# Performance work log

Measured on AMD Instinct MI355X. Metric: run time of the kernel, lower is better.

Reference implementation:

```python
import jax, jax.numpy as jnp
import numpy as np

N = 10000; IN = 256; HID = 256; Z = 64; NC = 10; E = 320000
GAMMA = -0.5; ZETA = 1.1; TEMP = 0.5  # GlobalArgs.gamma/zeta, AttentionFusion.temperature


def _spmm(row, col, vals, x):
    # sparse [N,N] @ dense [N,D] via gather + segment-sum scatter
    return jax.ops.segment_sum(vals[:, None] * x[col], row, num_segments=N)


def _encode(x, row, col, vals, gcn_W, gcn_b, m1_W, m1_b, m2_W, m2_b, s1_W, s1_b, s2_W, s2_b):
    hidden = jax.nn.relu(_spmm(row, col, vals, x @ gcn_W + gcn_b))  # GCNLayer
    mean = jax.nn.relu(hidden @ m1_W + m1_b) @ m2_W + m2_b
    std = jax.nn.softplus(jax.nn.relu(hidden @ s1_W + s1_b) @ s2_W + s2_b)
    return mean, mean, std  # eval mode: z = x_mean


def _denoise(x, row, col, vals, nb_W, nb_b, sf_W, sf_b, att_W, att_b):
    h1 = jax.nn.relu(x[row] @ nb_W + nb_b)  # nblayers_0 on source feats
    h2 = jax.nn.relu(x[col] @ sf_W + sf_b)  # selflayers_0 on dest feats
    w = jnp.concatenate([h1, h2], axis=1) @ att_W + att_b  # [E,1] log_alpha
    gate = jax.nn.sigmoid(w[:, 0])  # eval-mode hard-concrete
    mask = jnp.clip(gate * (ZETA - GAMMA) + GAMMA, 0.0, 1.0)
    mv = vals * mask
    rowsum = jax.ops.segment_sum(mv, row, num_segments=N) + 1e-10
    d = jnp.clip(rowsum ** -0.5, 0.0, 10.0)
    norm_vals = mv * d[row] * d[col]
    l0 = jnp.mean(jax.nn.sigmoid(w - jnp.log(-GAMMA / ZETA)))
    return norm_vals, l0


def setup_inputs() -> dict:
    key = jax.random.key(0)
    ks = jax.random.split(key, 32)
    w = lambda k, s: jax.random.normal(k, s, jnp.float32) * 0.05
    inp = {}
    inp['x'] = jax.random.normal(ks[0], (N, IN), jnp.float32)
    inp['row'] = jax.random.randint(ks[1], (E,), 0, N)
    inp['col'] = jax.random.randint(ks[2], (E,), 0, N)
    inp['adj_vals'] = jax.random.uniform(ks[3], (E,), jnp.float32)
    inp['gcn_W'] = w(ks[4], (IN, HID)); inp['gcn_b'] = jnp.zeros((HID,), jnp.float32)
    inp['m1_W'] = w(ks[5], (HID, Z)); inp['m1_b'] = jnp.zeros((Z,), jnp.float32)
    inp['m2_W'] = w(ks[6], (Z, Z)); inp['m2_b'] = jnp.zeros((Z,), jnp.float32)
    inp['s1_W'] = w(ks[7], (HID, Z)); inp['s1_b'] = jnp.zeros((Z,), jnp.float32)
    inp['s2_W'] = w(ks[8], (Z, Z)); inp['s2_b'] = jnp.zeros((Z,), jnp.float32)
    inp['nb_W'] = w(ks[9], (IN, HID)); inp['nb_b'] = jnp.zeros((HID,), jnp.float32)
    inp['sf_W'] = w(ks[10], (IN, HID)); inp['sf_b'] = jnp.zeros((HID,), jnp.float32)
    inp['att_W'] = w(ks[11], (2 * HID, 1)); inp['att_b'] = jnp.zeros((1,), jnp.float32)
    inp['f1_W'] = w(ks[12], (Z, 32)); inp['f1_b'] = jnp.zeros((32,), jnp.float32)
    inp['f2_W'] = jnp.zeros((32, 1), jnp.float32)  # att[2].weight.fill_(0.0)
    inp['head_W'] = w(ks[13], (Z, NC)); inp['head_b'] = jnp.zeros((NC,), jnp.float32)
    inp['d1_W'] = w(ks[14], (Z, HID)); inp['d1_b'] = jnp.zeros((HID,), jnp.float32)
    inp['d2_W'] = w(ks[15], (HID, IN)); inp['d2_b'] = jnp.zeros((IN,), jnp.float32)
    return inp


def reference(x, row, col, adj_vals, gcn_W, gcn_b, m1_W, m1_b, m2_W, m2_b, s1_W, s1_b, s2_W, s2_b,
              nb_W, nb_b, sf_W, sf_b, att_W, att_b, f1_W, f1_b, f2_W, head_W, head_b,
              d1_W, d1_b, d2_W, d2_b):
    enc = (gcn_W, gcn_b, m1_W, m1_b, m2_W, m2_b, s1_W, s1_b, s2_W, s2_b)
    # generative view
    z_gen, mu, logstd = _encode(x, row, col, adj_vals, *enc)
    adj_logits = z_gen @ z_gen.T  # vgae_decoder
    # denoised view
    den_vals, l0_loss = _denoise(x, row, col, adj_vals, nb_W, nb_b, sf_W, sf_b, att_W, att_b)
    z_den, _, _ = _encode(x, row, col, den_vals, *enc)
    # attention fusion
    h = jnp.stack([z_gen, z_den], axis=1)  # [N,2,Z]
    score = jnp.tanh(h @ f1_W + f1_b) @ f2_W  # [N,2,1]
    weights = jax.nn.softmax(score / TEMP, axis=1)
    z_fused = jnp.sum(h * weights, axis=1)
    # heads (cluster_proj is identity)
    q_fused = jax.nn.softmax(z_fused @ head_W + head_b, axis=1)
    q_gen = jax.nn.softmax(z_gen @ head_W + head_b, axis=1)
    q_den = jax.nn.softmax(z_den @ head_W + head_b, axis=1)
    recon_den = jax.nn.relu(z_den @ d1_W + d1_b) @ d2_W + d2_b
    return (q_fused, q_gen, q_den, adj_logits, z_fused, mu, logstd, l0_loss, z_den, weights, recon_den)
```

## Files before the change

kernel.cpp:

```cpp
#include <hip/hip_runtime.h>
#include <math.h>

#define NN 10000
#define EE 320000

#define OQF  0LL
#define OQG  100000LL
#define OQD  200000LL
#define OADJ 300000LL
#define OZF  100300000LL
#define OMU  100940000LL
#define OLS  101580000LL
#define OL0  102220000LL
#define OZD  102220001LL
#define OWT  102860001LL
#define OREC 102880001LL

typedef short short8 __attribute__((ext_vector_type(8)));
typedef float f32x4 __attribute__((ext_vector_type(4)));

static __device__ __forceinline__ ushort f2bf(float f) {
  uint u = __float_as_uint(f);
  return (ushort)((u + 0x7fffu + ((u >> 16) & 1u)) >> 16);
}

__global__ __launch_bounds__(256) void k_prep(
    const float* __restrict__ x,
    const float* __restrict__ gcnW, const float* __restrict__ nbW,
    const float* __restrict__ sfW, const float* __restrict__ d2W,
    const float* __restrict__ d1W, const float* __restrict__ m1W,
    const float* __restrict__ s1W, const float* __restrict__ m2W,
    const float* __restrict__ s2W,
    ushort* __restrict__ XB,
    ushort* __restrict__ GWT, ushort* __restrict__ NWT, ushort* __restrict__ SWT,
    ushort* __restrict__ D2T, ushort* __restrict__ D1T, ushort* __restrict__ M1T,
    ushort* __restrict__ S1T, ushort* __restrict__ M2T, ushort* __restrict__ S2T)
{
  const int b = blockIdx.x, tid = threadIdx.x;
  if (b < 2500) {
    const int i = b * 1024 + tid * 4;
    const float4 v = *(const float4*)(x + i);
    ushort4 u;
    u.x = f2bf(v.x); u.y = f2bf(v.y); u.z = f2bf(v.z); u.w = f2bf(v.w);
    *(ushort4*)(XB + i) = u;
    return;
  }
  const int t2 = b - 2500;
  if (t2 < 1024) {
    const int m = t2 >> 8, n = t2 & 255;
    const float* src = (m == 0) ? gcnW : (m == 1) ? nbW : (m == 2) ? sfW : d2W;
    ushort* dst = (m == 0) ? GWT : (m == 1) ? NWT : (m == 2) ? SWT : D2T;
    dst[n * 256 + tid] = f2bf(src[tid * 256 + n]);
  } else if (t2 < 1088) {
    const int local = (t2 - 1024) * 256 + tid;
    const int n = local >> 6, k = local & 63;
    D1T[local] = f2bf(d1W[k * 256 + n]);
  } else if (t2 < 1152) {
    const int n = t2 - 1088;
    M1T[n * 256 + tid] = f2bf(m1W[tid * 64 + n]);
  } else if (t2 < 1216) {
    const int n = t2 - 1152;
    S1T[n * 256 + tid] = f2bf(s1W[tid * 64 + n]);
  } else if (t2 < 1232) {
    const int local = (t2 - 1216) * 256 + tid;
    const int n = local >> 6, k = local & 63;
    M2T[local] = f2bf(m2W[k * 64 + n]);
  } else {
    const int local = (t2 - 1232) * 256 + tid;
    const int n = local >> 6, k = local & 63;
    S2T[local] = f2bf(s2W[k * 64 + n]);
  }
}

__global__ __launch_bounds__(256) void k_gin(
    const ushort* __restrict__ XB,
    const ushort* __restrict__ GWT, const ushort* __restrict__ NWT,
    const ushort* __restrict__ SWT,
    const float* __restrict__ gcnb, const float* __restrict__ nbb,
    const float* __restrict__ sfb, const float* __restrict__ attW,
    ushort* __restrict__ xwb, float* __restrict__ a1, float* __restrict__ a2)
{
  const int sel = blockIdx.y;
  const ushort* WT = (sel == 0) ? GWT : (sel == 1) ? NWT : SWT;
  const float* B = (sel == 0) ? gcnb : (sel == 1) ? nbb : sfb;
  const float* redw = attW + ((sel == 2) ? 256 : 0);
  float* redout = (sel == 1) ? a1 : a2;

  const int tid = threadIdx.x;
  const int wave = tid >> 6, lane = tid & 63;
  const int lr = lane & 15, lk = lane >> 4;
  const int i0 = blockIdx.x * 64;
  const int j0 = wave * 64;

  f32x4 acc[4][4];
#pragma unroll
  for (int ti = 0; ti < 4; ++ti)
#pragma unroll
    for (int tj = 0; tj < 4; ++tj) acc[ti][tj] = (f32x4){0.f, 0.f, 0.f, 0.f};

  const short8 z8 = {0, 0, 0, 0, 0, 0, 0, 0};
  for (int kk = 0; kk < 8; ++kk) {
    short8 a[4], bfr[4];
#pragma unroll
    for (int t = 0; t < 4; ++t) {
      const int ri = i0 + t * 16 + lr;
      a[t] = (ri < NN) ? *(const short8*)(XB + (size_t)ri * 256 + kk * 32 + lk * 8) : z8;
      bfr[t] = *(const short8*)(WT + (size_t)(j0 + t * 16 + lr) * 256 + kk * 32 + lk * 8);
    }
#pragma unroll
    for (int ti = 0; ti < 4; ++ti)
#pragma unroll
      for (int tj = 0; tj < 4; ++tj)
        acc[ti][tj] = __builtin_amdgcn_mfma_f32_16x16x32_bf16(a[ti], bfr[tj], acc[ti][tj], 0, 0, 0);
  }

  if (sel == 0) {
#pragma unroll
    for (int ti = 0; ti < 4; ++ti) {
      const int gi0 = i0 + ti * 16 + lk * 4;
#pragma unroll
      for (int tj = 0; tj < 4; ++tj) {
        const int gj = j0 + tj * 16 + lr;
        const float bv = B[gj];
#pragma unroll
        for (int r = 0; r < 4; ++r) {
          const int gi = gi0 + r;
          if (gi < NN) xwb[(size_t)gi * 256 + gj] = f2bf(acc[ti][tj][r] + bv);
        }
      }
    }
  } else {
    float bw[4], aw[4];
#pragma unroll
    for (int tj = 0; tj < 4; ++tj) {
      const int gj = j0 + tj * 16 + lr;
      bw[tj] = B[gj];
      aw[tj] = redw[gj];
    }
#pragma unroll
    for (int ti = 0; ti < 4; ++ti) {
      const int gi0 = i0 + ti * 16 + lk * 4;
#pragma unroll
      for (int r = 0; r < 4; ++r) {
        float s = 0.f;
#pragma unroll
        for (int tj = 0; tj < 4; ++tj)
          s += fmaxf(acc[ti][tj][r] + bw[tj], 0.f) * aw[tj];
#pragma unroll
        for (int m = 1; m < 16; m <<= 1) s += __shfl_xor(s, m, 64);
        const int gi = gi0 + r;
        if (lr == 0 && gi < NN) atomicAdd(&redout[gi], s);
      }
    }
  }
}

__global__ __launch_bounds__(256) void k_denoise(
    const int* __restrict__ row, const int* __restrict__ col,
    const float* __restrict__ vals, const float* __restrict__ a1,
    const float* __restrict__ a2, const float* __restrict__ attb,
    float4* __restrict__ bk, int* __restrict__ cnt, float* __restrict__ l0acc)
{
  const int e = blockIdx.x * 256 + threadIdx.x;
  const int r = row[e], c = col[e];
  const float w = a1[r] + a2[c] + attb[0];
  const float gate = 1.f / (1.f + expf(-w));
  const float mask = fminf(fmaxf(gate * 1.6f - 0.5f, 0.f), 1.f);
  const float m = vals[e] * mask;
  const int p = atomicAdd(&cnt[r], 1);
  if (p < 64) bk[(size_t)r * 64 + p] = make_float4(__int_as_float(c), vals[e], m, 0.f);
  float part = 1.f / (1.f + expf(-(w + 0.78845736f)));
#pragma unroll
  for (int off = 32; off > 0; off >>= 1) part += __shfl_down(part, off);
  __shared__ float sw[4];
  if ((threadIdx.x & 63) == 0) sw[threadIdx.x >> 6] = part;
  __syncthreads();
  if (threadIdx.x == 0) atomicAdd(l0acc, sw[0] + sw[1] + sw[2] + sw[3]);
}

__global__ __launch_bounds__(256) void k_dinv(
    const float4* __restrict__ bk, const int* __restrict__ cnt,
    float* __restrict__ dinv)
{
  const int tid = threadIdx.x;
  const int r = blockIdx.x * 4 + (tid >> 6);
  const int lane = tid & 63;
  if (r >= NN) return;
  const int m = min(cnt[r], 64);
  float s = (lane < m) ? bk[(size_t)r * 64 + lane].z : 0.f;
#pragma unroll
  for (int off = 32; off > 0; off >>= 1) s += __shfl_xor(s, off, 64);
  if (lane == 0) dinv[r] = fminf(rsqrtf(s + 1e-10f), 10.f);
}

__global__ __launch_bounds__(256) void k_spmm(
    const ushort* __restrict__ xwb, const float4* __restrict__ bk,
    const int* __restrict__ cnt, const float* __restrict__ dinv,
    ushort* __restrict__ h1, ushort* __restrict__ h2)
{
  const int tid = threadIdx.x;
  const int n = blockIdx.x * 2 + (tid >> 7);
  const int c = tid & 127;
  const int m = min(cnt[n], 64);
  const float dr = dinv[n];
  const float4* b = bk + (size_t)n * 64;
  float a10 = 0.f, a11 = 0.f, a20 = 0.f, a21 = 0.f;
  float b10 = 0.f, b11 = 0.f, b20 = 0.f, b21 = 0.f;
  int i = 0;
  for (; i + 2 <= m; i += 2) {
    const float4 e0 = b[i], e1 = b[i + 1];
    const int c0 = __float_as_int(e0.x), c1 = __float_as_int(e1.x);
    const uint u0 = *(const uint*)(xwb + (size_t)c0 * 256 + 2 * c);
    const uint u1 = *(const uint*)(xwb + (size_t)c1 * 256 + 2 * c);
    const float d0 = dr * dinv[c0] * e0.z;
    const float d1 = dr * dinv[c1] * e1.z;
    const float v00 = __uint_as_float(u0 << 16), v01 = __uint_as_float(u0 & 0xffff0000u);
    const float v10 = __uint_as_float(u1 << 16), v11 = __uint_as_float(u1 & 0xffff0000u);
    a10 = fmaf(e0.y, v00, a10); a11 = fmaf(e0.y, v01, a11);
    a20 = fmaf(d0, v00, a20);   a21 = fmaf(d0, v01, a21);
    b10 = fmaf(e1.y, v10, b10); b11 = fmaf(e1.y, v11, b11);
    b20 = fmaf(d1, v10, b20);   b21 = fmaf(d1, v11, b21);
  }
  if (i < m) {
    const float4 e0 = b[i];
    const int c0 = __float_as_int(e0.x);
    const uint u0 = *(const uint*)(xwb + (size_t)c0 * 256 + 2 * c);
    const float d0 = dr * dinv[c0] * e0.z;
    const float v00 = __uint_as_float(u0 << 16), v01 = __uint_as_float(u0 & 0xffff0000u);
    a10 = fmaf(e0.y, v00, a10); a11 = fmaf(e0.y, v01, a11);
    a20 = fmaf(d0, v00, a20);   a21 = fmaf(d0, v01, a21);
  }
  a10 += b10; a11 += b11; a20 += b20; a21 += b21;
  const uint p1 = (uint)f2bf(fmaxf(a10, 0.f)) | ((uint)f2bf(fmaxf(a11, 0.f)) << 16);
  const uint p2 = (uint)f2bf(fmaxf(a20, 0.f)) | ((uint)f2bf(fmaxf(a21, 0.f)) << 16);
  *(uint*)(h1 + (size_t)n * 256 + 2 * c) = p1;
  *(uint*)(h2 + (size_t)n * 256 + 2 * c) = p2;
}

__global__ __launch_bounds__(128) void k_tail(
    const ushort* __restrict__ H1B, const ushort* __restrict__ H2B,
    const ushort* __restrict__ M1T, const ushort* __restrict__ S1T,
    const ushort* __restrict__ M2T, const ushort* __restrict__ S2T,
    const float* __restrict__ m1b, const float* __restrict__ m2b,
    const float* __restrict__ s1b, const float* __restrict__ s2b,
    float* __restrict__ out, float* __restrict__ zden,
    ushort* __restrict__ zbg, ushort* __restrict__ zbd)
{
  const int v = blockIdx.y;
  const ushort* A   = (v == 2) ? H2B : H1B;
  const ushort* W1T = (v == 1) ? S1T : M1T;
  const float*  B1  = (v == 1) ? s1b : m1b;
  const ushort* W2T = (v == 1) ? S2T : M2T;
  const float*  B2  = (v == 1) ? s2b : m2b;

  __shared__ ushort Ts[128][72];
  const int tid = threadIdx.x;
  const int wave = tid >> 6, lane = tid & 63;
  const int lr = lane & 15, lk = lane >> 4;
  const int i0 = blockIdx.x * 128 + wave * 64;
  const short8 z8 = {0, 0, 0, 0, 0, 0, 0, 0};

  f32x4 acc[4][4];
#pragma unroll
  for (int ti = 0; ti < 4; ++ti)
#pragma unroll
    for (int tj = 0; tj < 4; ++tj) acc[ti][tj] = (f32x4){0.f, 0.f, 0.f, 0.f};
  for (int kk = 0; kk < 8; ++kk) {
    short8 a[4], bfr[4];
#pragma unroll
    for (int t = 0; t < 4; ++t) {
      const int ri = i0 + t * 16 + lr;
      a[t] = (ri < NN) ? *(const short8*)(A + (size_t)ri * 256 + kk * 32 + lk * 8) : z8;
      bfr[t] = *(const short8*)(W1T + (size_t)(t * 16 + lr) * 256 + kk * 32 + lk * 8);
    }
#pragma unroll
    for (int ti = 0; ti < 4; ++ti)
#pragma unroll
      for (int tj = 0; tj < 4; ++tj)
        acc[ti][tj] = __builtin_amdgcn_mfma_f32_16x16x32_bf16(a[ti], bfr[tj], acc[ti][tj], 0, 0, 0);
  }
#pragma unroll
  for (int ti = 0; ti < 4; ++ti) {
#pragma unroll
    for (int tj = 0; tj < 4; ++tj) {
      const int cl = tj * 16 + lr;
      const float b1 = B1[cl];
#pragma unroll
      for (int r = 0; r < 4; ++r) {
        const int lrow = wave * 64 + ti * 16 + lk * 4 + r;
        Ts[lrow][cl] = f2bf(fmaxf(acc[ti][tj][r] + b1, 0.f));
      }
    }
  }
  __syncthreads();
  f32x4 acc2[4][4];
#pragma unroll
  for (int ti = 0; ti < 4; ++ti)
#pragma unroll
    for (int tj = 0; tj < 4; ++tj) acc2[ti][tj] = (f32x4){0.f, 0.f, 0.f, 0.f};
  for (int kk = 0; kk < 2; ++kk) {
    short8 a[4], bfr[4];
#pragma unroll
    for (int t = 0; t < 4; ++t) {
      a[t] = *(const short8*)(&Ts[wave * 64 + t * 16 + lr][kk * 32 + lk * 8]);
      bfr[t] = *(const short8*)(W2T + (size_t)(t * 16 + lr) * 64 + kk * 32 + lk * 8);
    }
#pragma unroll
    for (int ti = 0; ti < 4; ++ti)
#pragma unroll
      for (int tj = 0; tj < 4; ++tj)
        acc2[ti][tj] = __builtin_amdgcn_mfma_f32_16x16x32_bf16(a[ti], bfr[tj], acc2[ti][tj], 0, 0, 0);
  }
#pragma unroll
  for (int ti = 0; ti < 4; ++ti) {
    const int gi0 = i0 + ti * 16 + lk * 4;
#pragma unroll
    for (int tj = 0; tj < 4; ++tj) {
      const int gj = tj * 16 + lr;
      const float bv = B2[gj];
#pragma unroll
      for (int r = 0; r < 4; ++r) {
        const int gi = gi0 + r;
        if (gi >= NN) continue;
        float t = acc2[ti][tj][r] + bv;
        if (v == 0) {
          out[OMU + (size_t)gi * 64 + gj] = t;
          zbg[(size_t)gi * 64 + gj] = f2bf(t);
        } else if (v == 1) {
          t = (t > 20.f) ? t : log1pf(expf(t));
          out[OLS + (size_t)gi * 64 + gj] = t;
        } else {
          zden[(size_t)gi * 64 + gj] = t;
          out[OZD + (size_t)gi * 64 + gj] = t;
          zbd[(size_t)gi * 64 + gj] = f2bf(t);
        }
      }
    }
  }
}

__global__ __launch_bounds__(256) void k_post(
    const ushort* __restrict__ ZBG, const ushort* __restrict__ ZBD,
    const float* __restrict__ ZDENW,
    const ushort* __restrict__ D1T, const float* __restrict__ d1b,
    const ushort* __restrict__ D2T, const float* __restrict__ d2b,
    const float* __restrict__ f1W, const float* __restrict__ f1b,
    const float* __restrict__ f2W,
    const float* __restrict__ hW, const float* __restrict__ hb,
    const float* __restrict__ l0acc, float* __restrict__ out)
{
  __shared__ char smraw[64 * 264 * 2];
  const int b = blockIdx.x;
  const int tid = threadIdx.x;
  const short8 z8 = {0, 0, 0, 0, 0, 0, 0, 0};

  if (b < 157) {
    ushort* HS = (ushort*)smraw;
    const int wave = tid >> 6, lane = tid & 63;
    const int lr = lane & 15, lk = lane >> 4;
    const int i0 = b * 64;
    const int j0 = wave * 64;
    f32x4 acc[4][4];
#pragma unroll
    for (int ti = 0; ti < 4; ++ti)
#pragma unroll
      for (int tj = 0; tj < 4; ++tj) acc[ti][tj] = (f32x4){0.f, 0.f, 0.f, 0.f};
    for (int kk = 0; kk < 2; ++kk) {
      short8 a[4], bfr[4];
#pragma unroll
      for (int t = 0; t < 4; ++t) {
        const int ri = i0 + t * 16 + lr;
        a[t] = (ri < NN) ? *(const short8*)(ZBD + (size_t)ri * 64 + kk * 32 + lk * 8) : z8;
        bfr[t] = *(const short8*)(D1T + (size_t)(j0 + t * 16 + lr) * 64 + kk * 32 + lk * 8);
      }
#pragma unroll
      for (int ti = 0; ti < 4; ++ti)
#pragma unroll
        for (int tj = 0; tj < 4; ++tj)
          acc[ti][tj] = __builtin_amdgcn_mfma_f32_16x16x32_bf16(a[ti], bfr[tj], acc[ti][tj], 0, 0, 0);
    }
#pragma unroll
    for (int ti = 0; ti < 4; ++ti) {
      const int rl0 = ti * 16 + lk * 4;
#pragma unroll
      for (int tj = 0; tj < 4; ++tj) {
        const int cl = j0 + tj * 16 + lr;
        const float bv = d1b[cl];
#pragma unroll
        for (int r = 0; r < 4; ++r)
          HS[(rl0 + r) * 264 + cl] = f2bf(fmaxf(acc[ti][tj][r] + bv, 0.f));
      }
    }
    __syncthreads();
#pragma unroll
    for (int ti = 0; ti < 4; ++ti)
#pragma unroll
      for (int tj = 0; tj < 4; ++tj) acc[ti][tj] = (f32x4){0.f, 0.f, 0.f, 0.f};
    for (int kk = 0; kk < 8; ++kk) {
      short8 a[4], bfr[4];
#pragma unroll
      for (int t = 0; t < 4; ++t) {
        a[t] = *(const short8*)(HS + (t * 16 + lr) * 264 + kk * 32 + lk * 8);
        bfr[t] = *(const short8*)(D2T + (size_t)(j0 + t * 16 + lr) * 256 + kk * 32 + lk * 8);
      }
#pragma unroll
      for (int ti = 0; ti < 4; ++ti)
#pragma unroll
        for (int tj = 0; tj < 4; ++tj)
          acc[ti][tj] = __builtin_amdgcn_mfma_f32_16x16x32_bf16(a[ti], bfr[tj], acc[ti][tj], 0, 0, 0);
    }
#pragma unroll
    for (int ti = 0; ti < 4; ++ti) {
      const int gi0 = i0 + ti * 16 + lk * 4;
#pragma unroll
      for (int tj = 0; tj < 4; ++tj) {
        const int gj = j0 + tj * 16 + lr;
        const float bv = d2b[gj];
#pragma unroll
        for (int r = 0; r < 4; ++r) {
          const int gi = gi0 + r;
          if (gi < NN) out[OREC + (size_t)gi * 256 + gj] = acc[ti][tj][r] + bv;
        }
      }
    }
  } else if (b < 197) {
    const int n = (b - 157) * 256 + tid;
    if (n == 0) out[OL0] = l0acc[0] * (1.f / (float)EE);
    if (n >= NN) return;
    const float* zg = out + OMU + (size_t)n * 64;
    const float* zdn = ZDENW + (size_t)n * 64;
    float ag[32], ad[32];
#pragma unroll
    for (int c2 = 0; c2 < 32; ++c2) { const float bb = f1b[c2]; ag[c2] = bb; ad[c2] = bb; }
    for (int l = 0; l < 64; ++l) {
      const float a = zg[l];
      const float d = zdn[l];
#pragma unroll
      for (int c2 = 0; c2 < 32; ++c2) {
        const float w = f1W[l * 32 + c2];
        ag[c2] = fmaf(a, w, ag[c2]);
        ad[c2] = fmaf(d, w, ad[c2]);
      }
    }
    float sg = 0.f, sd = 0.f;
#pragma unroll
    for (int c2 = 0; c2 < 32; ++c2) {
      sg += tanhf(ag[c2]) * f2W[c2];
      sd += tanhf(ad[c2]) * f2W[c2];
    }
    const float e0 = sg * 2.f, e1 = sd * 2.f;
    const float m = fmaxf(e0, e1);
    float w0 = expf(e0 - m), w1 = expf(e1 - m);
    const float inv = 1.f / (w0 + w1);
    w0 *= inv; w1 *= inv;
    float lgf[10], lgg[10], lgd[10];
#pragma unroll
    for (int c = 0; c < 10; ++c) { const float bb = hb[c]; lgf[c] = bb; lgg[c] = bb; lgd[c] = bb; }
    for (int l = 0; l < 64; ++l) {
      const float zgv = zg[l], zdv = zdn[l];
      const float zfv = w0 * zgv + w1 * zdv;
      out[OZF + (size_t)n * 64 + l] = zfv;
#pragma unroll
      for (int c = 0; c < 10; ++c) {
        const float w = hW[l * 10 + c];
        lgf[c] = fmaf(zfv, w, lgf[c]);
        lgg[c] = fmaf(zgv, w, lgg[c]);
        lgd[c] = fmaf(zdv, w, lgd[c]);
      }
    }
#pragma unroll
    for (int h = 0; h < 3; ++h) {
      float* lg = (h == 0) ? lgf : (h == 1) ? lgg : lgd;
      float* q = out + ((h == 0) ? OQF : (h == 1) ? OQG : OQD) + (size_t)n * 10;
      float mm = lg[0];
#pragma unroll
      for (int c = 1; c < 10; ++c) mm = fmaxf(mm, lg[c]);
      float s = 0.f;
#pragma unroll
      for (int c = 0; c < 10; ++c) { lg[c] = expf(lg[c] - mm); s += lg[c]; }
      const float invq = 1.f / s;
#pragma unroll
      for (int c = 0; c < 10; ++c) q[c] = lg[c] * invq;
    }
    out[OWT + (size_t)n * 2 + 0] = w0;
    out[OWT + (size_t)n * 2 + 1] = w1;
  } else {
    const int bb = b - 197;
    const int bi = bb / 79, bj = bb % 79;
    const int wave = tid >> 6, lane = tid & 63;
    const int lr = lane & 15, lk = lane >> 4;
    const int i0 = bi * 128 + (wave >> 1) * 64;
    const int j0 = bj * 128 + (wave & 1) * 64;
    float* zs = (float*)smraw + wave * (16 * 76);
    short8 a[4][2], bfr[4][2];
#pragma unroll
    for (int t = 0; t < 4; ++t) {
      const int ri = i0 + t * 16 + lr;
      const int rj = j0 + t * 16 + lr;
#pragma unroll
      for (int kk = 0; kk < 2; ++kk) {
        a[t][kk] = (ri < NN) ? *(const short8*)(ZBG + (size_t)ri * 64 + kk * 32 + lk * 8) : z8;
        bfr[t][kk] = (rj < NN) ? *(const short8*)(ZBG + (size_t)rj * 64 + kk * 32 + lk * 8) : z8;
      }
    }
    f32x4 acc[4][4];
#pragma unroll
    for (int ti = 0; ti < 4; ++ti)
#pragma unroll
      for (int tj = 0; tj < 4; ++tj) {
        acc[ti][tj] = (f32x4){0.f, 0.f, 0.f, 0.f};
        acc[ti][tj] = __builtin_amdgcn_mfma_f32_16x16x32_bf16(a[ti][0], bfr[tj][0], acc[ti][tj], 0, 0, 0);
        acc[ti][tj] = __builtin_amdgcn_mfma_f32_16x16x32_bf16(a[ti][1], bfr[tj][1], acc[ti][tj], 0, 0, 0);
      }
#pragma unroll
    for (int ti = 0; ti < 4; ++ti) {
#pragma unroll
      for (int tj = 0; tj < 4; ++tj)
#pragma unroll
        for (int r = 0; r < 4; ++r)
          zs[(lk * 4 + r) * 76 + tj * 16 + lr] = acc[ti][tj][r];
#pragma unroll
      for (int s = 0; s < 4; ++s) {
        const int rrow = (s & 1) * 8 + (lane >> 3);
        const int ccol = (s >> 1) * 32 + (lane & 7) * 4;
        const int gi = i0 + ti * 16 + rrow;
        const int gj = j0 + ccol;
        if (gi < NN && gj < NN) {
          float4 v;
          v.x = zs[rrow * 76 + ccol + 0];
          v.y = zs[rrow * 76 + ccol + 1];
          v.z = zs[rrow * 76 + ccol + 2];
          v.w = zs[rrow * 76 + ccol + 3];
          *(float4*)(out + OADJ + (size_t)gi * NN + gj) = v;
        }
      }
    }
  }
}

extern "C" void kernel_launch(void* const* d_in, const int* in_sizes, int n_in,
                              void* d_out, int out_size, void* d_ws, size_t ws_size,
                              hipStream_t stream)
{
  const float* x     = (const float*)d_in[0];
  const int*   row   = (const int*)d_in[1];
  const int*   col   = (const int*)d_in[2];
  const float* avals = (const float*)d_in[3];
  const float* gcnW  = (const float*)d_in[4];
  const float* gcnb  = (const float*)d_in[5];
  const float* m1W   = (const float*)d_in[6];
  const float* m1b   = (const float*)d_in[7];
  const float* m2W   = (const float*)d_in[8];
  const float* m2b   = (const float*)d_in[9];
  const float* s1W   = (const float*)d_in[10];
  const float* s1b   = (const float*)d_in[11];
  const float* s2W   = (const float*)d_in[12];
  const float* s2b   = (const float*)d_in[13];
  const float* nbW   = (const float*)d_in[14];
  const float* nbb   = (const float*)d_in[15];
  const float* sfW   = (const float*)d_in[16];
  const float* sfb   = (const float*)d_in[17];
  const float* attW  = (const float*)d_in[18];
  const float* attb  = (const float*)d_in[19];
  const float* f1W   = (const float*)d_in[20];
  const float* f1b   = (const float*)d_in[21];
  const float* f2W   = (const float*)d_in[22];
  const float* headW = (const float*)d_in[23];
  const float* headb = (const float*)d_in[24];
  const float* d1W   = (const float*)d_in[25];
  const float* d1b   = (const float*)d_in[26];
  const float* d2W   = (const float*)d_in[27];
  const float* d2b   = (const float*)d_in[28];
  float* out = (float*)d_out;

  float* ws = (float*)d_ws;
  size_t o = 0;
  float4* BK   = (float4*)(ws + o); o += (size_t)NN * 64 * 4;
  ushort* XB   = (ushort*)(ws + o); o += (size_t)NN * 128;
  ushort* XWB  = (ushort*)(ws + o); o += (size_t)NN * 128;
  ushort* GWT  = (ushort*)(ws + o); o += 32768;
  ushort* NWT  = (ushort*)(ws + o); o += 32768;
  ushort* SWT  = (ushort*)(ws + o); o += 32768;
  ushort* D2T  = (ushort*)(ws + o); o += 32768;
  ushort* D1T  = (ushort*)(ws + o); o += 8192;
  ushort* M1T  = (ushort*)(ws + o); o += 8192;
  ushort* S1T  = (ushort*)(ws + o); o += 8192;
  ushort* M2T  = (ushort*)(ws + o); o += 2048;
  ushort* S2T  = (ushort*)(ws + o); o += 2048;
  ushort* H1B  = (ushort*)(ws + o); o += (size_t)NN * 128;
  ushort* H2B  = (ushort*)(ws + o); o += (size_t)NN * 128;
  float* ZDENW = ws + o; o += (size_t)NN * 64;
  ushort* ZBG  = (ushort*)(ws + o); o += (size_t)NN * 32;
  ushort* ZBD  = (ushort*)(ws + o); o += (size_t)NN * 32;
  float* DINV  = ws + o; o += NN;
  const size_t zoff = o;
  float* A1    = ws + o; o += NN;
  float* A2    = ws + o; o += NN;
  int*   CNT   = (int*)(ws + o); o += NN;
  float* L0A   = ws + o; o += 1;

  hipMemsetAsync((void*)(ws + zoff), 0, (o - zoff) * sizeof(float), stream);

  k_prep<<<3748, 256, 0, stream>>>(x, gcnW, nbW, sfW, d2W, d1W, m1W, s1W, m2W, s2W,
                                   XB, GWT, NWT, SWT, D2T, D1T, M1T, S1T, M2T, S2T);
  k_gin<<<dim3(157, 3), 256, 0, stream>>>(XB, GWT, NWT, SWT, gcnb, nbb, sfb, attW, XWB, A1, A2);
  k_denoise<<<EE / 256, 256, 0, stream>>>(row, col, avals, A1, A2, attb, BK, CNT, L0A);
  k_dinv<<<2500, 256, 0, stream>>>(BK, CNT, DINV);
  k_spmm<<<NN / 2, 256, 0, stream>>>(XWB, BK, CNT, DINV, H1B, H2B);
  k_tail<<<dim3(79, 3), 128, 0, stream>>>(H1B, H2B, M1T, S1T, M2T, S2T,
                                          m1b, m2b, s1b, s2b, out, ZDENW, ZBG, ZBD);
  k_post<<<6438, 256, 0, stream>>>(ZBG, ZBD, ZDENW, D1T, d1b, D2T, d2b,
                                   f1W, f1b, f2W, headW, headb, L0A, out);
}
```

Before: 283.0 us.

## Fuse all stages into one persistent kernel with grid-wide barriers

Replaces the seven separate kernel launches with a single persistent kernel of 512 blocks that loops over each stage's virtual blocks and separates stages with an atomic-counter grid barrier. The aim is to remove per-launch overhead and the idle tails between dependent kernels. In exchange, each stage is limited to 512 resident blocks, spin-wait barriers add their own cost, and correctness depends on all 512 blocks being co-resident.

```diff
diff --git a/kernel.cpp b/kernel.cpp
--- a/kernel.cpp
+++ b/kernel.cpp
@@ -3,6 +3,7 @@
 
 #define NN 10000
 #define EE 320000
+#define NB 512
 
 #define OQF  0LL
 #define OQG  100000LL
@@ -24,374 +25,99 @@
   return (ushort)((u + 0x7fffu + ((u >> 16) & 1u)) >> 16);
 }
 
-__global__ __launch_bounds__(256) void k_prep(
-    const float* __restrict__ x,
-    const float* __restrict__ gcnW, const float* __restrict__ nbW,
-    const float* __restrict__ sfW, const float* __restrict__ d2W,
-    const float* __restrict__ d1W, const float* __restrict__ m1W,
-    const float* __restrict__ s1W, const float* __restrict__ m2W,
-    const float* __restrict__ s2W,
-    ushort* __restrict__ XB,
+static __device__ __forceinline__ void gbar(int* ctr) {
+  __syncthreads();
+  if (threadIdx.x == 0) {
+    __threadfence();
+    __hip_atomic_fetch_add(ctr, 1, __ATOMIC_ACQ_REL, __HIP_MEMORY_SCOPE_AGENT);
+    while (__hip_atomic_load(ctr, __ATOMIC_ACQUIRE, __HIP_MEMORY_SCOPE_AGENT) < NB) {
+      __builtin_amdgcn_s_sleep(1);
+    }
+    __threadfence();
+  }
+  __syncthreads();
+}
+
+__global__ __launch_bounds__(256, 2) void k_fused(
+    const float* __restrict__ x, const int* __restrict__ row,
+    const int* __restrict__ col, const float* __restrict__ avals,
+    const float* __restrict__ gcnW, const float* __restrict__ gcnb,
+    const float* __restrict__ m1W, const float* __restrict__ m1b,
+    const float* __restrict__ m2W, const float* __restrict__ m2b,
+    const float* __restrict__ s1W, const float* __restrict__ s1b,
+    const float* __restrict__ s2W, const float* __restrict__ s2b,
+    const float* __restrict__ nbW, const float* __restrict__ nbb,
+    const float* __restrict__ sfW, const float* __restrict__ sfb,
+    const float* __restrict__ attW, const float* __restrict__ attb,
+    const float* __restrict__ f1W, const float* __restrict__ f1b,
+    const float* __restrict__ f2W, const float* __restrict__ hW,
+    const float* __restrict__ hb,
+    const float* __restrict__ d1W, const float* __restrict__ d1b,
+    const float* __restrict__ d2W, const float* __restrict__ d2b,
+    float* __restrict__ out,
+    float4* __restrict__ BK, ushort* __restrict__ XB, ushort* __restrict__ XWB,
     ushort* __restrict__ GWT, ushort* __restrict__ NWT, ushort* __restrict__ SWT,
     ushort* __restrict__ D2T, ushort* __restrict__ D1T, ushort* __restrict__ M1T,
-    ushort* __restrict__ S1T, ushort* __restrict__ M2T, ushort* __restrict__ S2T)
+    ushort* __restrict__ S1T, ushort* __restrict__ M2T, ushort* __restrict__ S2T,
+    ushort* __restrict__ H1B, ushort* __restrict__ H2B,
+    float* __restrict__ ZDENW, ushort* __restrict__ ZBG, ushort* __restrict__ ZBD,
+    float* __restrict__ DINV, float* __restrict__ A1, float* __restrict__ A2,
+    int* __restrict__ CNT, float* __restrict__ L0A, int* __restrict__ BAR)
 {
-  const int b = blockIdx.x, tid = threadIdx.x;
-  if (b < 2500) {
-    const int i = b * 1024 + tid * 4;
-    const float4 v = *(const float4*)(x + i);
-    ushort4 u;
-    u.x = f2bf(v.x); u.y = f2bf(v.y); u.z = f2bf(v.z); u.w = f2bf(v.w);
-    *(ushort4*)(XB + i) = u;
-    return;
-  }
-  const int t2 = b - 2500;
-  if (t2 < 1024) {
-    const int m = t2 >> 8, n = t2 & 255;
-    const float* src = (m == 0) ? gcnW : (m == 1) ? nbW : (m == 2) ? sfW : d2W;
-    ushort* dst = (m == 0) ? GWT : (m == 1) ? NWT : (m == 2) ? SWT : D2T;
-    dst[n * 256 + tid] = f2bf(src[tid * 256 + n]);
-  } else if (t2 < 1088) {
-    const int local = (t2 - 1024) * 256 + tid;
-    const int n = local >> 6, k = local & 63;
-    D1T[local] = f2bf(d1W[k * 256 + n]);
-  } else if (t2 < 1152) {
-    const int n = t2 - 1088;
-    M1T[n * 256 + tid] = f2bf(m1W[tid * 64 + n]);
-  } else if (t2 < 1216) {
-    const int n = t2 - 1152;
-    S1T[n * 256 + tid] = f2bf(s1W[tid * 64 + n]);
-  } else if (t2 < 1232) {
-    const int local = (t2 - 1216) * 256 + tid;
-    const int n = local >> 6, k = local & 63;
-    M2T[local] = f2bf(m2W[k * 64 + n]);
-  } else {
-    const int local = (t2 - 1232) * 256 + tid;
-    const int n = local >> 6, k = local & 63;
-    S2T[local] = f2bf(s2W[k * 64 + n]);
-  }
-}
-
-__global__ __launch_bounds__(256) void k_gin(
-    const ushort* __restrict__ XB,
-    const ushort* __restrict__ GWT, const ushort* __restrict__ NWT,
-    const ushort* __restrict__ SWT,
-    const float* __restrict__ gcnb, const float* __restrict__ nbb,
-    const float* __restrict__ sfb, const float* __restrict__ attW,
-    ushort* __restrict__ xwb, float* __restrict__ a1, float* __restrict__ a2)
-{
-  const int sel = blockIdx.y;
-  const ushort* WT = (sel == 0) ? GWT : (sel == 1) ? NWT : SWT;
-  const float* B = (sel == 0) ? gcnb : (sel == 1) ? nbb : sfb;
-  const float* redw = attW + ((sel == 2) ? 256 : 0);
-  float* redout = (sel == 1) ? a1 : a2;
-
-  const int tid = threadIdx.x;
-  const int wave = tid >> 6, lane = tid & 63;
-  const int lr = lane & 15, lk = lane >> 4;
-  const int i0 = blockIdx.x * 64;
-  const int j0 = wave * 64;
-
-  f32x4 acc[4][4];
-#pragma unroll
-  for (int ti = 0; ti < 4; ++ti)
-#pragma unroll
-    for (int tj = 0; tj < 4; ++tj) acc[ti][tj] = (f32x4){0.f, 0.f, 0.f, 0.f};
-
-  const short8 z8 = {0, 0, 0, 0, 0, 0, 0, 0};
-  for (int kk = 0; kk < 8; ++kk) {
-    short8 a[4], bfr[4];
-#pragma unroll
-    for (int t = 0; t < 4; ++t) {
-      const int ri = i0 + t * 16 + lr;
-      a[t] = (ri < NN) ? *(const short8*)(XB + (size_t)ri * 256 + kk * 32 + lk * 8) : z8;
-      bfr[t] = *(const short8*)(WT + (size_t)(j0 + t * 16 + lr) * 256 + kk * 32 + lk * 8);
-    }
-#pragma unroll
-    for (int ti = 0; ti < 4; ++ti)
-#pragma unroll
-      for (int tj = 0; tj < 4; ++tj)
-        acc[ti][tj] = __builtin_amdgcn_mfma_f32_16x16x32_bf16(a[ti], bfr[tj], acc[ti][tj], 0, 0, 0);
-  }
-
-  if (sel == 0) {
-#pragma unroll
-    for (int ti = 0; ti < 4; ++ti) {
-      const int gi0 = i0 + ti * 16 + lk * 4;
-#pragma unroll
-      for (int tj = 0; tj < 4; ++tj) {
-        const int gj = j0 + tj * 16 + lr;
-        const float bv = B[gj];
-#pragma unroll
-        for (int r = 0; r < 4; ++r) {
-          const int gi = gi0 + r;
-          if (gi < NN) xwb[(size_t)gi * 256 + gj] = f2bf(acc[ti][tj][r] + bv);
-        }
-      }
-    }
-  } else {
-    float bw[4], aw[4];
-#pragma unroll
-    for (int tj = 0; tj < 4; ++tj) {
-      const int gj = j0 + tj * 16 + lr;
-      bw[tj] = B[gj];
-      aw[tj] = redw[gj];
-    }
-#pragma unroll
-    for (int ti = 0; ti < 4; ++ti) {
-      const int gi0 = i0 + ti * 16 + lk * 4;
-#pragma unroll
-      for (int r = 0; r < 4; ++r) {
-        float s = 0.f;
-#pragma unroll
-        for (int tj = 0; tj < 4; ++tj)
-          s += fmaxf(acc[ti][tj][r] + bw[tj], 0.f) * aw[tj];
-#pragma unroll
-        for (int m = 1; m < 16; m <<= 1) s += __shfl_xor(s, m, 64);
-        const int gi = gi0 + r;
-        if (lr == 0 && gi < NN) atomicAdd(&redout[gi], s);
-      }
-    }
-  }
-}
-
-__global__ __launch_bounds__(256) void k_denoise(
-    const int* __restrict__ row, const int* __restrict__ col,
-    const float* __restrict__ vals, const float* __restrict__ a1,
-    const float* __restrict__ a2, const float* __restrict__ attb,
-    float4* __restrict__ bk, int* __restrict__ cnt, float* __restrict__ l0acc)
-{
-  const int e = blockIdx.x * 256 + threadIdx.x;
-  const int r = row[e], c = col[e];
-  const float w = a1[r] + a2[c] + attb[0];
-  const float gate = 1.f / (1.f + expf(-w));
-  const float mask = fminf(fmaxf(gate * 1.6f - 0.5f, 0.f), 1.f);
-  const float m = vals[e] * mask;
-  const int p = atomicAdd(&cnt[r], 1);
-  if (p < 64) bk[(size_t)r * 64 + p] = make_float4(__int_as_float(c), vals[e], m, 0.f);
-  float part = 1.f / (1.f + expf(-(w + 0.78845736f)));
-#pragma unroll
-  for (int off = 32; off > 0; off >>= 1) part += __shfl_down(part, off);
+  __shared__ char smraw[256 * 72 * 2];
   __shared__ float sw[4];
-  if ((threadIdx.x & 63) == 0) sw[threadIdx.x >> 6] = part;
-  __syncthreads();
-  if (threadIdx.x == 0) atomicAdd(l0acc, sw[0] + sw[1] + sw[2] + sw[3]);
-}
-
-__global__ __launch_bounds__(256) void k_dinv(
-    const float4* __restrict__ bk, const int* __restrict__ cnt,
-    float* __restrict__ dinv)
-{
-  const int tid = threadIdx.x;
-  const int r = blockIdx.x * 4 + (tid >> 6);
-  const int lane = tid & 63;
-  if (r >= NN) return;
-  const int m = min(cnt[r], 64);
-  float s = (lane < m) ? bk[(size_t)r * 64 + lane].z : 0.f;
-#pragma unroll
-  for (int off = 32; off > 0; off >>= 1) s += __shfl_xor(s, off, 64);
-  if (lane == 0) dinv[r] = fminf(rsqrtf(s + 1e-10f), 10.f);
-}
-
-__global__ __launch_bounds__(256) void k_spmm(
-    const ushort* __restrict__ xwb, const float4* __restrict__ bk,
-    const int* __restrict__ cnt, const float* __restrict__ dinv,
-    ushort* __restrict__ h1, ushort* __restrict__ h2)
-{
-  const int tid = threadIdx.x;
-  const int n = blockIdx.x * 2 + (tid >> 7);
-  const int c = tid & 127;
-  const int m = min(cnt[n], 64);
-  const float dr = dinv[n];
-  const float4* b = bk + (size_t)n * 64;
-  float a10 = 0.f, a11 = 0.f, a20 = 0.f, a21 = 0.f;
-  float b10 = 0.f, b11 = 0.f, b20 = 0.f, b21 = 0.f;
-  int i = 0;
-  for (; i + 2 <= m; i += 2) {
-    const float4 e0 = b[i], e1 = b[i + 1];
-    const int c0 = __float_as_int(e0.x), c1 = __float_as_int(e1.x);
-    const uint u0 = *(const uint*)(xwb + (size_t)c0 * 256 + 2 * c);
-    const uint u1 = *(const uint*)(xwb + (size_t)c1 * 256 + 2 * c);
-    const float d0 = dr * dinv[c0] * e0.z;
-    const float d1 = dr * dinv[c1] * e1.z;
-    const float v00 = __uint_as_float(u0 << 16), v01 = __uint_as_float(u0 & 0xffff0000u);
-    const float v10 = __uint_as_float(u1 << 16), v11 = __uint_as_float(u1 & 0xffff0000u);
-    a10 = fmaf(e0.y, v00, a10); a11 = fmaf(e0.y, v01, a11);
-    a20 = fmaf(d0, v00, a20);   a21 = fmaf(d0, v01, a21);
-    b10 = fmaf(e1.y, v10, b10); b11 = fmaf(e1.y, v11, b11);
-    b20 = fmaf(d1, v10, b20);   b21 = fmaf(d1, v11, b21);
-  }
-  if (i < m) {
-    const float4 e0 = b[i];
-    const int c0 = __float_as_int(e0.x);
-    const uint u0 = *(const uint*)(xwb + (size_t)c0 * 256 + 2 * c);
-    const float d0 = dr * dinv[c0] * e0.z;
-    const float v00 = __uint_as_float(u0 << 16), v01 = __uint_as_float(u0 & 0xffff0000u);
-    a10 = fmaf(e0.y, v00, a10); a11 = fmaf(e0.y, v01, a11);
-    a20 = fmaf(d0, v00, a20);   a21 = fmaf(d0, v01, a21);
-  }
-  a10 += b10; a11 += b11; a20 += b20; a21 += b21;
-  const uint p1 = (uint)f2bf(fmaxf(a10, 0.f)) | ((uint)f2bf(fmaxf(a11, 0.f)) << 16);
-  const uint p2 = (uint)f2bf(fmaxf(a20, 0.f)) | ((uint)f2bf(fmaxf(a21, 0.f)) << 16);
-  *(uint*)(h1 + (size_t)n * 256 + 2 * c) = p1;
-  *(uint*)(h2 + (size_t)n * 256 + 2 * c) = p2;
-}
-
-__global__ __launch_bounds__(128) void k_tail(
-    const ushort* __restrict__ H1B, const ushort* __restrict__ H2B,
-    const ushort* __restrict__ M1T, const ushort* __restrict__ S1T,
-    const ushort* __restrict__ M2T, const ushort* __restrict__ S2T,
-    const float* __restrict__ m1b, const float* __restrict__ m2b,
-    const float* __restrict__ s1b, const float* __restrict__ s2b,
-    float* __restrict__ out, float* __restrict__ zden,
-    ushort* __restrict__ zbg, ushort* __restrict__ zbd)
-{
-  const int v = blockIdx.y;
-  const ushort* A   = (v == 2) ? H2B : H1B;
-  const ushort* W1T = (v == 1) ? S1T : M1T;
-  const float*  B1  = (v == 1) ? s1b : m1b;
-  const ushort* W2T = (v == 1) ? S2T : M2T;
-  const float*  B2  = (v == 1) ? s2b : m2b;
-
-  __shared__ ushort Ts[128][72];
-  const int tid = threadIdx.x;
-  const int wave = tid >> 6, lane = tid & 63;
-  const int lr = lane & 15, lk = lane >> 4;
-  const int i0 = blockIdx.x * 128 + wave * 64;
-  const short8 z8 = {0, 0, 0, 0, 0, 0, 0, 0};
-
-  f32x4 acc[4][4];
-#pragma unroll
-  for (int ti = 0; ti < 4; ++ti)
-#pragma unroll
-    for (int tj = 0; tj < 4; ++tj) acc[ti][tj] = (f32x4){0.f, 0.f, 0.f, 0.f};
-  for (int kk = 0; kk < 8; ++kk) {
-    short8 a[4], bfr[4];
-#pragma unroll
-    for (int t = 0; t < 4; ++t) {
-      const int ri = i0 + t * 16 + lr;
-      a[t] = (ri < NN) ? *(const short8*)(A + (size_t)ri * 256 + kk * 32 + lk * 8) : z8;
-      bfr[t] = *(const short8*)(W1T + (size_t)(t * 16 + lr) * 256 + kk * 32 + lk * 8);
-    }
-#pragma unroll
-    for (int ti = 0; ti < 4; ++ti)
-#pragma unroll
-      for (int tj = 0; tj < 4; ++tj)
-        acc[ti][tj] = __builtin_amdgcn_mfma_f32_16x16x32_bf16(a[ti], bfr[tj], acc[ti][tj], 0, 0, 0);
-  }
-#pragma unroll
-  for (int ti = 0; ti < 4; ++ti) {
-#pragma unroll
-    for (int tj = 0; tj < 4; ++tj) {
-      const int cl = tj * 16 + lr;
-      const float b1 = B1[cl];
-#pragma unroll
-      for (int r = 0; r < 4; ++r) {
-        const int lrow = wave * 64 + ti * 16 + lk * 4 + r;
-        Ts[lrow][cl] = f2bf(fmaxf(acc[ti][tj][r] + b1, 0.f));
-      }
-    }
-  }
-  __syncthreads();
-  f32x4 acc2[4][4];
-#pragma unroll
-  for (int ti = 0; ti < 4; ++ti)
-#pragma unroll
-    for (int tj = 0; tj < 4; ++tj) acc2[ti][tj] = (f32x4){0.f, 0.f, 0.f, 0.f};
-  for (int kk = 0; kk < 2; ++kk) {
-    short8 a[4], bfr[4];
-#pragma unroll
-    for (int t = 0; t < 4; ++t) {
-      a[t] = *(const short8*)(&Ts[wave * 64 + t * 16 + lr][kk * 32 + lk * 8]);
-      bfr[t] = *(const short8*)(W2T + (size_t)(t * 16 + lr) * 64 + kk * 32 + lk * 8);
-    }
-#pragma unroll
-    for (int ti = 0; ti < 4; ++ti)
-#pragma unroll
-      for (int tj = 0; tj < 4; ++tj)
-        acc2[ti][tj] = __builtin_amdgcn_mfma_f32_16x16x32_bf16(a[ti], bfr[tj], acc2[ti][tj], 0, 0, 0);
-  }
-#pragma unroll
-  for (int ti = 0; ti < 4; ++ti) {
-    const int gi0 = i0 + ti * 16 + lk * 4;
-#pragma unroll
-    for (int tj = 0; tj < 4; ++tj) {
-      const int gj = tj * 16 + lr;
-      const float bv = B2[gj];
-#pragma unroll
-      for (int r = 0; r < 4; ++r) {
-        const int gi = gi0 + r;
-        if (gi >= NN) continue;
-        float t = acc2[ti][tj][r] + bv;
-        if (v == 0) {
-          out[OMU + (size_t)gi * 64 + gj] = t;
-          zbg[(size_t)gi * 64 + gj] = f2bf(t);
-        } else if (v == 1) {
-          t = (t > 20.f) ? t : log1pf(expf(t));
-          out[OLS + (size_t)gi * 64 + gj] = t;
-        } else {
-          zden[(size_t)gi * 64 + gj] = t;
-          out[OZD + (size_t)gi * 64 + gj] = t;
-          zbd[(size_t)gi * 64 + gj] = f2bf(t);
-        }
-      }
-    }
-  }
-}
-
-__global__ __launch_bounds__(256) void k_post(
-    const ushort* __restrict__ ZBG, const ushort* __restrict__ ZBD,
-    const float* __restrict__ ZDENW,
-    const ushort* __restrict__ D1T, const float* __restrict__ d1b,
-    const ushort* __restrict__ D2T, const float* __restrict__ d2b,
-    const float* __restrict__ f1W, const float* __restrict__ f1b,
-    const float* __restrict__ f2W,
-    const float* __restrict__ hW, const float* __restrict__ hb,
-    const float* __restrict__ l0acc, float* __restrict__ out)
-{
-  __shared__ char smraw[64 * 264 * 2];
-  const int b = blockIdx.x;
+  const int bid = blockIdx.x;
   const int tid = threadIdx.x;
   const short8 z8 = {0, 0, 0, 0, 0, 0, 0, 0};
 
-  if (b < 157) {
-    ushort* HS = (ushort*)smraw;
+  for (int vb = bid; vb < 3748; vb += NB) {
+    if (vb < 2500) {
+      const int i = vb * 1024 + tid * 4;
+      const float4 v = *(const float4*)(x + i);
+      ushort4 u;
+      u.x = f2bf(v.x); u.y = f2bf(v.y); u.z = f2bf(v.z); u.w = f2bf(v.w);
+      *(ushort4*)(XB + i) = u;
+      continue;
+    }
+    const int t2 = vb - 2500;
+    if (t2 < 1024) {
+      const int m = t2 >> 8, n = t2 & 255;
+      const float* src = (m == 0) ? gcnW : (m == 1) ? nbW : (m == 2) ? sfW : d2W;
+      ushort* dst = (m == 0) ? GWT : (m == 1) ? NWT : (m == 2) ? SWT : D2T;
+      dst[n * 256 + tid] = f2bf(src[tid * 256 + n]);
+    } else if (t2 < 1088) {
+      const int local = (t2 - 1024) * 256 + tid;
+      const int n = local >> 6, k = local & 63;
+      D1T[local] = f2bf(d1W[k * 256 + n]);
+    } else if (t2 < 1152) {
+      const int n = t2 - 1088;
+      M1T[n * 256 + tid] = f2bf(m1W[tid * 64 + n]);
+    } else if (t2 < 1216) {
+      const int n = t2 - 1152;
+      S1T[n * 256 + tid] = f2bf(s1W[tid * 64 + n]);
+    } else if (t2 < 1232) {
+      const int local = (t2 - 1216) * 256 + tid;
+      const int n = local >> 6, k = local & 63;
+      M2T[local] = f2bf(m2W[k * 64 + n]);
+    } else {
+      const int local = (t2 - 1232) * 256 + tid;
+      const int n = local >> 6, k = local & 63;
+      S2T[local] = f2bf(s2W[k * 64 + n]);
+    }
+  }
+  gbar(BAR + 0);
+
+  for (int vb = bid; vb < 471; vb += NB) {
+    const int bx = vb % 157, sel = vb / 157;
+    const ushort* WT = (sel == 0) ? GWT : (sel == 1) ? NWT : SWT;
+    const float* B = (sel == 0) ? gcnb : (sel == 1) ? nbb : sfb;
+    const float* redw = attW + ((sel == 2) ? 256 : 0);
+    float* redout = (sel == 1) ? A1 : A2;
     const int wave = tid >> 6, lane = tid & 63;
     const int lr = lane & 15, lk = lane >> 4;
-    const int i0 = b * 64;
+    const int i0 = bx * 64;
     const int j0 = wave * 64;
     f32x4 acc[4][4];
-#pragma unroll
-    for (int ti = 0; ti < 4; ++ti)
-#pragma unroll
-      for (int tj = 0; tj < 4; ++tj) acc[ti][tj] = (f32x4){0.f, 0.f, 0.f, 0.f};
-    for (int kk = 0; kk < 2; ++kk) {
-      short8 a[4], bfr[4];
-#pragma unroll
-      for (int t = 0; t < 4; ++t) {
-        const int ri = i0 + t * 16 + lr;
-        a[t] = (ri < NN) ? *(const short8*)(ZBD + (size_t)ri * 64 + kk * 32 + lk * 8) : z8;
-        bfr[t] = *(const short8*)(D1T + (size_t)(j0 + t * 16 + lr) * 64 + kk * 32 + lk * 8);
-      }
-#pragma unroll
-      for (int ti = 0; ti < 4; ++ti)
-#pragma unroll
-        for (int tj = 0; tj < 4; ++tj)
-          acc[ti][tj] = __builtin_amdgcn_mfma_f32_16x16x32_bf16(a[ti], bfr[tj], acc[ti][tj], 0, 0, 0);
-    }
-#pragma unroll
-    for (int ti = 0; ti < 4; ++ti) {
-      const int rl0 = ti * 16 + lk * 4;
-#pragma unroll
-      for (int tj = 0; tj < 4; ++tj) {
-        const int cl = j0 + tj * 16 + lr;
-        const float bv = d1b[cl];
-#pragma unroll
-        for (int r = 0; r < 4; ++r)
-          HS[(rl0 + r) * 264 + cl] = f2bf(fmaxf(acc[ti][tj][r] + bv, 0.f));
-      }
-    }
-    __syncthreads();
 #pragma unroll
     for (int ti = 0; ti < 4; ++ti)
 #pragma unroll
@@ -400,8 +126,9 @@
       short8 a[4], bfr[4];
 #pragma unroll
       for (int t = 0; t < 4; ++t) {
-        a[t] = *(const short8*)(HS + (t * 16 + lr) * 264 + kk * 32 + lk * 8);
-        bfr[t] = *(const short8*)(D2T + (size_t)(j0 + t * 16 + lr) * 256 + kk * 32 + lk * 8);
+        const int ri = i0 + t * 16 + lr;
+        a[t] = (ri < NN) ? *(const short8*)(XB + (size_t)ri * 256 + kk * 32 + lk * 8) : z8;
+        bfr[t] = *(const short8*)(WT + (size_t)(j0 + t * 16 + lr) * 256 + kk * 32 + lk * 8);
       }
 #pragma unroll
       for (int ti = 0; ti < 4; ++ti)
@@ -409,129 +136,394 @@
         for (int tj = 0; tj < 4; ++tj)
           acc[ti][tj] = __builtin_amdgcn_mfma_f32_16x16x32_bf16(a[ti], bfr[tj], acc[ti][tj], 0, 0, 0);
     }
+    if (sel == 0) {
+#pragma unroll
+      for (int ti = 0; ti < 4; ++ti) {
+        const int gi0 = i0 + ti * 16 + lk * 4;
+#pragma unroll
+        for (int tj = 0; tj < 4; ++tj) {
+          const int gj = j0 + tj * 16 + lr;
+          const float bv = B[gj];
+#pragma unroll
+          for (int r = 0; r < 4; ++r) {
+            const int gi = gi0 + r;
+            if (gi < NN) XWB[(size_t)gi * 256 + gj] = f2bf(acc[ti][tj][r] + bv);
+          }
+        }
+      }
+    } else {
+      float bw[4], aw[4];
+#pragma unroll
+      for (int tj = 0; tj < 4; ++tj) {
+        const int gj = j0 + tj * 16 + lr;
+        bw[tj] = B[gj];
+        aw[tj] = redw[gj];
+      }
+#pragma unroll
+      for (int ti = 0; ti < 4; ++ti) {
+        const int gi0 = i0 + ti * 16 + lk * 4;
+#pragma unroll
+        for (int r = 0; r < 4; ++r) {
+          float s = 0.f;
+#pragma unroll
+          for (int tj = 0; tj < 4; ++tj)
+            s += fmaxf(acc[ti][tj][r] + bw[tj], 0.f) * aw[tj];
+#pragma unroll
+          for (int m = 1; m < 16; m <<= 1) s += __shfl_xor(s, m, 64);
+          const int gi = gi0 + r;
+          if (lr == 0 && gi < NN) atomicAdd(&redout[gi], s);
+        }
+      }
+    }
+  }
+  gbar(BAR + 1);
+
+  for (int vb = bid; vb < 1250; vb += NB) {
+    const int e = vb * 256 + tid;
+    const int r = row[e], c = col[e];
+    const float w = A1[r] + A2[c] + attb[0];
+    const float gate = 1.f / (1.f + expf(-w));
+    const float mask = fminf(fmaxf(gate * 1.6f - 0.5f, 0.f), 1.f);
+    const float m = avals[e] * mask;
+    const int p = atomicAdd(&CNT[r], 1);
+    if (p < 64) BK[(size_t)r * 64 + p] = make_float4(__int_as_float(c), avals[e], m, 0.f);
+    float part = 1.f / (1.f + expf(-(w + 0.78845736f)));
+#pragma unroll
+    for (int off = 32; off > 0; off >>= 1) part += __shfl_down(part, off);
+    if ((tid & 63) == 0) sw[tid >> 6] = part;
+    __syncthreads();
+    if (tid == 0) atomicAdd(L0A, sw[0] + sw[1] + sw[2] + sw[3]);
+    __syncthreads();
+  }
+  gbar(BAR + 2);
+
+  for (int vb = bid; vb < 2500; vb += NB) {
+    const int r = vb * 4 + (tid >> 6);
+    const int lane = tid & 63;
+    if (r < NN) {
+      const int m = min(CNT[r], 64);
+      float s = (lane < m) ? BK[(size_t)r * 64 + lane].z : 0.f;
+#pragma unroll
+      for (int off = 32; off > 0; off >>= 1) s += __shfl_xor(s, off, 64);
+      if (lane == 0) DINV[r] = fminf(rsqrtf(s + 1e-10f), 10.f);
+    }
+  }
+  gbar(BAR + 3);
+
+  for (int vb = bid; vb < 5000; vb += NB) {
+    const int n = vb * 2 + (tid >> 7);
+    const int c = tid & 127;
+    const int m = min(CNT[n], 64);
+    const float dr = DINV[n];
+    const float4* b = BK + (size_t)n * 64;
+    float a10 = 0.f, a11 = 0.f, a20 = 0.f, a21 = 0.f;
+    float b10 = 0.f, b11 = 0.f, b20 = 0.f, b21 = 0.f;
+    int i = 0;
+    for (; i + 2 <= m; i += 2) {
+      const float4 e0 = b[i], e1 = b[i + 1];
+      const int c0 = __float_as_int(e0.x), c1 = __float_as_int(e1.x);
+      const uint u0 = *(const uint*)(XWB + (size_t)c0 * 256 + 2 * c);
+      const uint u1 = *(const uint*)(XWB + (size_t)c1 * 256 + 2 * c);
+      const float d0 = dr * DINV[c0] * e0.z;
+      const float d1 = dr * DINV[c1] * e1.z;
+      const float v00 = __uint_as_float(u0 << 16), v01 = __uint_as_float(u0 & 0xffff0000u);
+      const float v10 = __uint_as_float(u1 << 16), v11 = __uint_as_float(u1 & 0xffff0000u);
+      a10 = fmaf(e0.y, v00, a10); a11 = fmaf(e0.y, v01, a11);
+      a20 = fmaf(d0, v00, a20);   a21 = fmaf(d0, v01, a21);
+      b10 = fmaf(e1.y, v10, b10); b11 = fmaf(e1.y, v11, b11);
+      b20 = fmaf(d1, v10, b20);   b21 = fmaf(d1, v11, b21);
+    }
+    if (i < m) {
+      const float4 e0 = b[i];
+      const int c0 = __float_as_int(e0.x);
+      const uint u0 = *(const uint*)(XWB + (size_t)c0 * 256 + 2 * c);
+      const float d0 = dr * DINV[c0] * e0.z;
+      const float v00 = __uint_as_float(u0 << 16), v01 = __uint_as_float(u0 & 0xffff0000u);
+      a10 = fmaf(e0.y, v00, a10); a11 = fmaf(e0.y, v01, a11);
+      a20 = fmaf(d0, v00, a20);   a21 = fmaf(d0, v01, a21);
+    }
+    a10 += b10; a11 += b11; a20 += b20; a21 += b21;
+    const uint p1 = (uint)f2bf(fmaxf(a10, 0.f)) | ((uint)f2bf(fmaxf(a11, 0.f)) << 16);
+    const uint p2 = (uint)f2bf(fmaxf(a20, 0.f)) | ((uint)f2bf(fmaxf(a21, 0.f)) << 16);
+    *(uint*)(H1B + (size_t)n * 256 + 2 * c) = p1;
+    *(uint*)(H2B + (size_t)n * 256 + 2 * c) = p2;
+  }
+  gbar(BAR + 4);
+
+  for (int vb = bid; vb < 120; vb += NB) {
+    const int bx = vb % 40, v = vb / 40;
+    const ushort* A   = (v == 2) ? H2B : H1B;
+    const ushort* W1T = (v == 1) ? S1T : M1T;
+    const float*  B1  = (v == 1) ? s1b : m1b;
+    const ushort* W2T = (v == 1) ? S2T : M2T;
+    const float*  B2  = (v == 1) ? s2b : m2b;
+    ushort* Ts = (ushort*)smraw;
+    const int wave = tid >> 6, lane = tid & 63;
+    const int lr = lane & 15, lk = lane >> 4;
+    const int i0 = bx * 256 + wave * 64;
+
+    f32x4 acc[4][4];
+#pragma unroll
+    for (int ti = 0; ti < 4; ++ti)
+#pragma unroll
+      for (int tj = 0; tj < 4; ++tj) acc[ti][tj] = (f32x4){0.f, 0.f, 0.f, 0.f};
+    for (int kk = 0; kk < 8; ++kk) {
+      short8 a[4], bfr[4];
+#pragma unroll
+      for (int t = 0; t < 4; ++t) {
+        const int ri = i0 + t * 16 + lr;
+        a[t] = (ri < NN) ? *(const short8*)(A + (size_t)ri * 256 + kk * 32 + lk * 8) : z8;
+        bfr[t] = *(const short8*)(W1T + (size_t)(t * 16 + lr) * 256 + kk * 32 + lk * 8);
+      }
+#pragma unroll
+      for (int ti = 0; ti < 4; ++ti)
+#pragma unroll
+        for (int tj = 0; tj < 4; ++tj)
+          acc[ti][tj] = __builtin_amdgcn_mfma_f32_16x16x32_bf16(a[ti], bfr[tj], acc[ti][tj], 0, 0, 0);
+    }
+#pragma unroll
+    for (int ti = 0; ti < 4; ++ti) {
+#pragma unroll
+      for (int tj = 0; tj < 4; ++tj) {
+        const int cl = tj * 16 + lr;
+        const float b1 = B1[cl];
+#pragma unroll
+        for (int r = 0; r < 4; ++r) {
+          const int lrow = wave * 64 + ti * 16 + lk * 4 + r;
+          Ts[lrow * 72 + cl] = f2bf(fmaxf(acc[ti][tj][r] + b1, 0.f));
+        }
+      }
+    }
+    __syncthreads();
+    f32x4 acc2[4][4];
+#pragma unroll
+    for (int ti = 0; ti < 4; ++ti)
+#pragma unroll
+      for (int tj = 0; tj < 4; ++tj) acc2[ti][tj] = (f32x4){0.f, 0.f, 0.f, 0.f};
+    for (int kk = 0; kk < 2; ++kk) {
+      short8 a[4], bfr[4];
+#pragma unroll
+      for (int t = 0; t < 4; ++t) {
+        a[t] = *(const short8*)(&Ts[(wave * 64 + t * 16 + lr) * 72 + kk * 32 + lk * 8]);
+        bfr[t] = *(const short8*)(W2T + (size_t)(t * 16 + lr) * 64 + kk * 32 + lk * 8);
+      }
+#pragma unroll
+      for (int ti = 0; ti < 4; ++ti)
+#pragma unroll
+        for (int tj = 0; tj < 4; ++tj)
+          acc2[ti][tj] = __builtin_amdgcn_mfma_f32_16x16x32_bf16(a[ti], bfr[tj], acc2[ti][tj], 0, 0, 0);
+    }
 #pragma unroll
     for (int ti = 0; ti < 4; ++ti) {
       const int gi0 = i0 + ti * 16 + lk * 4;
 #pragma unroll
       for (int tj = 0; tj < 4; ++tj) {
-        const int gj = j0 + tj * 16 + lr;
-        const float bv = d2b[gj];
+        const int gj = tj * 16 + lr;
+        const float bv = B2[gj];
 #pragma unroll
         for (int r = 0; r < 4; ++r) {
           const int gi = gi0 + r;
-          if (gi < NN) out[OREC + (size_t)gi * 256 + gj] = acc[ti][tj][r] + bv;
-        }
-      }
-    }
-  } else if (b < 197) {
-    const int n = (b - 157) * 256 + tid;
-    if (n == 0) out[OL0] = l0acc[0] * (1.f / (float)EE);
-    if (n >= NN) return;
-    const float* zg = out + OMU + (size_t)n * 64;
-    const float* zdn = ZDENW + (size_t)n * 64;
-    float ag[32], ad[32];
-#pragma unroll
-    for (int c2 = 0; c2 < 32; ++c2) { const float bb = f1b[c2]; ag[c2] = bb; ad[c2] = bb; }
-    for (int l = 0; l < 64; ++l) {
-      const float a = zg[l];
-      const float d = zdn[l];
+          if (gi >= NN) continue;
+          float t = acc2[ti][tj][r] + bv;
+          if (v == 0) {
+            out[OMU + (size_t)gi * 64 + gj] = t;
+            ZBG[(size_t)gi * 64 + gj] = f2bf(t);
+          } else if (v == 1) {
+            t = (t > 20.f) ? t : log1pf(expf(t));
+            out[OLS + (size_t)gi * 64 + gj] = t;
+          } else {
+            ZDENW[(size_t)gi * 64 + gj] = t;
+            out[OZD + (size_t)gi * 64 + gj] = t;
+            ZBD[(size_t)gi * 64 + gj] = f2bf(t);
+          }
+        }
+      }
+    }
+    __syncthreads();
+  }
+  gbar(BAR + 5);
+
+  for (int vb = bid; vb < 6438; vb += NB) {
+    if (vb < 157) {
+      ushort* HS = (ushort*)smraw;
+      const int wave = tid >> 6, lane = tid & 63;
+      const int lr = lane & 15, lk = lane >> 4;
+      const int i0 = vb * 64;
+      const int j0 = wave * 64;
+      f32x4 acc[4][4];
+#pragma unroll
+      for (int ti = 0; ti < 4; ++ti)
+#pragma unroll
+        for (int tj = 0; tj < 4; ++tj) acc[ti][tj] = (f32x4){0.f, 0.f, 0.f, 0.f};
+      for (int kk = 0; kk < 2; ++kk) {
+        short8 a[4], bfr[4];
+#pragma unroll
+        for (int t = 0; t < 4; ++t) {
+          const int ri = i0 + t * 16 + lr;
+          a[t] = (ri < NN) ? *(const short8*)(ZBD + (size_t)ri * 64 + kk * 32 + lk * 8) : z8;
+          bfr[t] = *(const short8*)(D1T + (size_t)(j0 + t * 16 + lr) * 64 + kk * 32 + lk * 8);
+        }
+#pragma unroll
+        for (int ti = 0; ti < 4; ++ti)
+#pragma unroll
+          for (int tj = 0; tj < 4; ++tj)
+            acc[ti][tj] = __builtin_amdgcn_mfma_f32_16x16x32_bf16(a[ti], bfr[tj], acc[ti][tj], 0, 0, 0);
+      }
+#pragma unroll
+      for (int ti = 0; ti < 4; ++ti) {
+        const int rl0 = ti * 16 + lk * 4;
+#pragma unroll
+        for (int tj = 0; tj < 4; ++tj) {
+          const int cl = j0 + tj * 16 + lr;
+          const float bv = d1b[cl];
+#pragma unroll
+          for (int r = 0; r < 4; ++r)
+            HS[(rl0 + r) * 264 + cl] = f2bf(fmaxf(acc[ti][tj][r] + bv, 0.f));
+        }
+      }
+      __syncthreads();
+#pragma unroll
+      for (int ti = 0; ti < 4; ++ti)
+#pragma unroll
+        for (int tj = 0; tj < 4; ++tj) acc[ti][tj] = (f32x4){0.f, 0.f, 0.f, 0.f};
+      for (int kk = 0; kk < 8; ++kk) {
+        short8 a[4], bfr[4];
+#pragma unroll
+        for (int t = 0; t < 4; ++t) {
+          a[t] = *(const short8*)(HS + (t * 16 + lr) * 264 + kk * 32 + lk * 8);
+          bfr[t] = *(const short8*)(D2T + (size_t)(j0 + t * 16 + lr) * 256 + kk * 32 + lk * 8);
+        }
+#pragma unroll
+        for (int ti = 0; ti < 4; ++ti)
+#pragma unroll
+          for (int tj = 0; tj < 4; ++tj)
+            acc[ti][tj] = __builtin_amdgcn_mfma_f32_16x16x32_bf16(a[ti], bfr[tj], acc[ti][tj], 0, 0, 0);
+      }
+#pragma unroll
+      for (int ti = 0; ti < 4; ++ti) {
+        const int gi0 = i0 + ti * 16 + lk * 4;
+#pragma unroll
+        for (int tj = 0; tj < 4; ++tj) {
+          const int gj = j0 + tj * 16 + lr;
+          const float bv = d2b[gj];
+#pragma unroll
+          for (int r = 0; r < 4; ++r) {
+            const int gi = gi0 + r;
+            if (gi < NN) out[OREC + (size_t)gi * 256 + gj] = acc[ti][tj][r] + bv;
+          }
+        }
+      }
+      __syncthreads();
+    } else if (vb < 197) {
+      const int n = (vb - 157) * 256 + tid;
+      if (n == 0) out[OL0] = L0A[0] * (1.f / (float)EE);
+      if (n >= NN) continue;
+      const float* zg = out + OMU + (size_t)n * 64;
+      const float* zdn = ZDENW + (size_t)n * 64;
+      float ag[32], ad[32];
+#pragma unroll
+      for (int c2 = 0; c2 < 32; ++c2) { const float bb = f1b[c2]; ag[c2] = bb; ad[c2] = bb; }
+      for (int l = 0; l < 64; ++l) {
+        const float a = zg[l];
+        const float d = zdn[l];
+#pragma unroll
+        for (int c2 = 0; c2 < 32; ++c2) {
+          const float w = f1W[l * 32 + c2];
+          ag[c2] = fmaf(a, w, ag[c2]);
+          ad[c2] = fmaf(d, w, ad[c2]);
+        }
+      }
+      float sg = 0.f, sd = 0.f;
 #pragma unroll
       for (int c2 = 0; c2 < 32; ++c2) {
-        const float w = f1W[l * 32 + c2];
-        ag[c2] = fmaf(a, w, ag[c2]);
-        ad[c2] = fmaf(d, w, ad[c2]);
-      }
-    }
-    float sg = 0.f, sd = 0.f;
-#pragma unroll
-    for (int c2 = 0; c2 < 32; ++c2) {
-      sg += tanhf(ag[c2]) * f2W[c2];
-      sd += tanhf(ad[c2]) * f2W[c2];
-    }
-    const float e0 = sg * 2.f, e1 = sd * 2.f;
-    const float m = fmaxf(e0, e1);
-    float w0 = expf(e0 - m), w1 = expf(e1 - m);
-    const float inv = 1.f / (w0 + w1);
-    w0 *= inv; w1 *= inv;
-    float lgf[10], lgg[10], lgd[10];
-#pragma unroll
-    for (int c = 0; c < 10; ++c) { const float bb = hb[c]; lgf[c] = bb; lgg[c] = bb; lgd[c] = bb; }
-    for (int l = 0; l < 64; ++l) {
-      const float zgv = zg[l], zdv = zdn[l];
-      const float zfv = w0 * zgv + w1 * zdv;
-      out[OZF + (size_t)n * 64 + l] = zfv;
-#pragma unroll
-      for (int c = 0; c < 10; ++c) {
-        const float w = hW[l * 10 + c];
-        lgf[c] = fmaf(zfv, w, lgf[c]);
-        lgg[c] = fmaf(zgv, w, lgg[c]);
-        lgd[c] = fmaf(zdv, w, lgd[c]);
-      }
-    }
-#pragma unroll
-    for (int h = 0; h < 3; ++h) {
-      float* lg = (h == 0) ? lgf : (h == 1) ? lgg : lgd;
-      float* q = out + ((h == 0) ? OQF : (h == 1) ? OQG : OQD) + (size_t)n * 10;
-      float mm = lg[0];
-#pragma unroll
-      for (int c = 1; c < 10; ++c) mm = fmaxf(mm, lg[c]);
-      float s = 0.f;
-#pragma unroll
-      for (int c = 0; c < 10; ++c) { lg[c] = expf(lg[c] - mm); s += lg[c]; }
-      const float invq = 1.f / s;
-#pragma unroll
-      for (int c = 0; c < 10; ++c) q[c] = lg[c] * invq;
-    }
-    out[OWT + (size_t)n * 2 + 0] = w0;
-    out[OWT + (size_t)n * 2 + 1] = w1;
-  } else {
-    const int bb = b - 197;
-    const int bi = bb / 79, bj = bb % 79;
-    const int wave = tid >> 6, lane = tid & 63;
-    const int lr = lane & 15, lk = lane >> 4;
-    const int i0 = bi * 128 + (wave >> 1) * 64;
-    const int j0 = bj * 128 + (wave & 1) * 64;
-    float* zs = (float*)smraw + wave * (16 * 76);
-    short8 a[4][2], bfr[4][2];
-#pragma unroll
-    for (int t = 0; t < 4; ++t) {
-      const int ri = i0 + t * 16 + lr;
-      const int rj = j0 + t * 16 + lr;
-#pragma unroll
-      for (int kk = 0; kk < 2; ++kk) {
-        a[t][kk] = (ri < NN) ? *(const short8*)(ZBG + (size_t)ri * 64 + kk * 32 + lk * 8) : z8;
-        bfr[t][kk] = (rj < NN) ? *(const short8*)(ZBG + (size_t)rj * 64 + kk * 32 + lk * 8) : z8;
-      }
-    }
-    f32x4 acc[4][4];
-#pragma unroll
-    for (int ti = 0; ti < 4; ++ti)
-#pragma unroll
-      for (int tj = 0; tj < 4; ++tj) {
-        acc[ti][tj] = (f32x4){0.f, 0.f, 0.f, 0.f};
-        acc[ti][tj] = __builtin_amdgcn_mfma_f32_16x16x32_bf16(a[ti][0], bfr[tj][0], acc[ti][tj], 0, 0, 0);
-        acc[ti][tj] = __builtin_amdgcn_mfma_f32_16x16x32_bf16(a[ti][1], bfr[tj][1], acc[ti][tj], 0, 0, 0);
-      }
-#pragma unroll
-    for (int ti = 0; ti < 4; ++ti) {
-#pragma unroll
-      for (int tj = 0; tj < 4; ++tj)
-#pragma unroll
-        for (int r = 0; r < 4; ++r)
-          zs[(lk * 4 + r) * 76 + tj * 16 + lr] = acc[ti][tj][r];
-#pragma unroll
-      for (int s = 0; s < 4; ++s) {
-        const int rrow = (s & 1) * 8 + (lane >> 3);
-        const int ccol = (s >> 1) * 32 + (lane & 7) * 4;
-        const int gi = i0 + ti * 16 + rrow;
-        const int gj = j0 + ccol;
-        if (gi < NN && gj < NN) {
-          float4 v;
-          v.x = zs[rrow * 76 + ccol + 0];
-          v.y = zs[rrow * 76 + ccol + 1];
-          v.z = zs[rrow * 76 + ccol + 2];
-          v.w = zs[rrow * 76 + ccol + 3];
-          *(float4*)(out + OADJ + (size_t)gi * NN + gj) = v;
+        sg += tanhf(ag[c2]) * f2W[c2];
+        sd += tanhf(ad[c2]) * f2W[c2];
+      }
+      const float e0 = sg * 2.f, e1 = sd * 2.f;
+      const float m = fmaxf(e0, e1);
+      float w0 = expf(e0 - m), w1 = expf(e1 - m);
+      const float inv = 1.f / (w0 + w1);
+      w0 *= inv; w1 *= inv;
+      float lgf[10], lgg[10], lgd[10];
+#pragma unroll
+      for (int c2 = 0; c2 < 10; ++c2) { const float bb = hb[c2]; lgf[c2] = bb; lgg[c2] = bb; lgd[c2] = bb; }
+      for (int l = 0; l < 64; ++l) {
+        const float zgv = zg[l], zdv = zdn[l];
+        const float zfv = w0 * zgv + w1 * zdv;
+        out[OZF + (size_t)n * 64 + l] = zfv;
+#pragma unroll
+        for (int c2 = 0; c2 < 10; ++c2) {
+          const float w = hW[l * 10 + c2];
+          lgf[c2] = fmaf(zfv, w, lgf[c2]);
+          lgg[c2] = fmaf(zgv, w, lgg[c2]);
+          lgd[c2] = fmaf(zdv, w, lgd[c2]);
+        }
+      }
+#pragma unroll
+      for (int h = 0; h < 3; ++h) {
+        float* lg = (h == 0) ? lgf : (h == 1) ? lgg : lgd;
+        float* q = out + ((h == 0) ? OQF : (h == 1) ? OQG : OQD) + (size_t)n * 10;
+        float mm = lg[0];
+#pragma unroll
+        for (int c2 = 1; c2 < 10; ++c2) mm = fmaxf(mm, lg[c2]);
+        float s = 0.f;
+#pragma unroll
+        for (int c2 = 0; c2 < 10; ++c2) { lg[c2] = expf(lg[c2] - mm); s += lg[c2]; }
+        const float invq = 1.f / s;
+#pragma unroll
+        for (int c2 = 0; c2 < 10; ++c2) q[c2] = lg[c2] * invq;
+      }
+      out[OWT + (size_t)n * 2 + 0] = w0;
+      out[OWT + (size_t)n * 2 + 1] = w1;
+    } else {
+      const int bb = vb - 197;
+      const int bi = bb / 79, bj = bb % 79;
+      const int wave = tid >> 6, lane = tid & 63;
+      const int lr = lane & 15, lk = lane >> 4;
+      const int i0 = bi * 128 + (wave >> 1) * 64;
+      const int j0 = bj * 128 + (wave & 1) * 64;
+      float* zs = (float*)smraw + wave * (16 * 76);
+      short8 a[4][2], bfr[4][2];
+#pragma unroll
+      for (int t = 0; t < 4; ++t) {
+        const int ri = i0 + t * 16 + lr;
+        const int rj = j0 + t * 16 + lr;
+#pragma unroll
+        for (int kk = 0; kk < 2; ++kk) {
+          a[t][kk] = (ri < NN) ? *(const short8*)(ZBG + (size_t)ri * 64 + kk * 32 + lk * 8) : z8;
+          bfr[t][kk] = (rj < NN) ? *(const short8*)(ZBG + (size_t)rj * 64 + kk * 32 + lk * 8) : z8;
+        }
+      }
+      f32x4 acc[4][4];
+#pragma unroll
+      for (int ti = 0; ti < 4; ++ti)
+#pragma unroll
+        for (int tj = 0; tj < 4; ++tj) {
+          acc[ti][tj] = (f32x4){0.f, 0.f, 0.f, 0.f};
+          acc[ti][tj] = __builtin_amdgcn_mfma_f32_16x16x32_bf16(a[ti][0], bfr[tj][0], acc[ti][tj], 0, 0, 0);
+          acc[ti][tj] = __builtin_amdgcn_mfma_f32_16x16x32_bf16(a[ti][1], bfr[tj][1], acc[ti][tj], 0, 0, 0);
+        }
+#pragma unroll
+      for (int ti = 0; ti < 4; ++ti) {
+#pragma unroll
+        for (int tj = 0; tj < 4; ++tj)
+#pragma unroll
+          for (int r = 0; r < 4; ++r)
+            zs[(lk * 4 + r) * 76 + tj * 16 + lr] = acc[ti][tj][r];
+#pragma unroll
+        for (int s = 0; s < 4; ++s) {
+          const int rrow = (s & 1) * 8 + (lane >> 3);
+          const int ccol = (s >> 1) * 32 + (lane & 7) * 4;
+          const int gi = i0 + ti * 16 + rrow;
+          const int gj = j0 + ccol;
+          if (gi < NN && gj < NN) {
+            float4 v;
+            v.x = zs[rrow * 76 + ccol + 0];
+            v.y = zs[rrow * 76 + ccol + 1];
+            v.z = zs[rrow * 76 + ccol + 2];
+            v.w = zs[rrow * 76 + ccol + 3];
+            *(float4*)(out + OADJ + (size_t)gi * NN + gj) = v;
+          }
         }
       }
     }
@@ -598,17 +590,14 @@
   float* A2    = ws + o; o += NN;
   int*   CNT   = (int*)(ws + o); o += NN;
   float* L0A   = ws + o; o += 1;
+  int*   BAR   = (int*)(ws + o); o += 8;
 
   hipMemsetAsync((void*)(ws + zoff), 0, (o - zoff) * sizeof(float), stream);
 
-  k_prep<<<3748, 256, 0, stream>>>(x, gcnW, nbW, sfW, d2W, d1W, m1W, s1W, m2W, s2W,
-                                   XB, GWT, NWT, SWT, D2T, D1T, M1T, S1T, M2T, S2T);
-  k_gin<<<dim3(157, 3), 256, 0, stream>>>(XB, GWT, NWT, SWT, gcnb, nbb, sfb, attW, XWB, A1, A2);
-  k_denoise<<<EE / 256, 256, 0, stream>>>(row, col, avals, A1, A2, attb, BK, CNT, L0A);
-  k_dinv<<<2500, 256, 0, stream>>>(BK, CNT, DINV);
-  k_spmm<<<NN / 2, 256, 0, stream>>>(XWB, BK, CNT, DINV, H1B, H2B);
-  k_tail<<<dim3(79, 3), 128, 0, stream>>>(H1B, H2B, M1T, S1T, M2T, S2T,
-                                          m1b, m2b, s1b, s2b, out, ZDENW, ZBG, ZBD);
-  k_post<<<6438, 256, 0, stream>>>(ZBG, ZBD, ZDENW, D1T, d1b, D2T, d2b,
-                                   f1W, f1b, f2W, headW, headb, L0A, out);
+  k_fused<<<NB, 256, 0, stream>>>(
+      x, row, col, avals, gcnW, gcnb, m1W, m1b, m2W, m2b, s1W, s1b, s2W, s2b,
+      nbW, nbb, sfW, sfb, attW, attb, f1W, f1b, f2W, headW, headb,
+      d1W, d1b, d2W, d2b, out,
+      BK, XB, XWB, GWT, NWT, SWT, D2T, D1T, M1T, S1T, M2T, S2T,
+      H1B, H2B, ZDENW, ZBG, ZBD, DINV, A1, A2, CNT, L0A, BAR);
 }
```

Result: slower. 1.058 ms (+273.8%).
